# Performance work log

Measured on AMD Instinct MI355X. Metric: run time of the kernel, lower is better.

Reference implementation:

```python
import jax, jax.numpy as jnp
import numpy as np
import itertools

DIM = 7
N_H2, N_H3 = 21, 77

def _perm_sign(p):
    inv = sum(1 for i in range(len(p)) for j in range(i + 1, len(p)) if p[i] > p[j])
    return -1.0 if inv % 2 else 1.0

def _build_wedge_constants():
    # C[a,b,c] = sign of (pair_a, pair_b, triple_c) as a permutation of (0..6),
    # zero unless the 2+2+3 indices are disjoint (coefficient of the volume form
    # in omega_a ^ omega_b ^ Phi_c on ordered-multi-index components).
    idx2 = list(itertools.combinations(range(DIM), 2))   # 21 ordered pairs
    idx3 = list(itertools.combinations(range(DIM), 3))   # 35 ordered triples
    C = np.zeros((len(idx2), len(idx2), len(idx3)), dtype=np.float32)
    for a, pa in enumerate(idx2):
        sa = set(pa)
        for b, pb in enumerate(idx2):
            if sa & set(pb):
                continue
            sab = sa | set(pb)
            for c, pc in enumerate(idx3):
                full = pa + pb + pc
                if sab.isdisjoint(pc):
                    C[a, b, c] = _perm_sign(full)
    return jnp.asarray(C)

C_WEDGE = _build_wedge_constants()  # (21, 21, 35), sparse structure constants

def setup_inputs() -> dict:
    key = jax.random.key(0)
    k1, k2, k3 = jax.random.split(key, 3)
    batch = 4096
    omega = jax.random.normal(k1, (batch, N_H2, 21), dtype=jnp.float32)
    Phi = jax.random.normal(k2, (batch, N_H3, 35), dtype=jnp.float32)
    metric = jax.random.normal(k3, (batch, DIM, DIM), dtype=jnp.float32)
    return {"omega": omega, "Phi": Phi, "metric": metric}

def reference(omega, Phi, metric):
    # Monte-Carlo volume weights, normalized (normalize=True path)
    vol = jnp.sqrt(jnp.abs(jnp.linalg.det(metric)))        # (n,)
    w = vol / vol.sum()
    # Fused triple wedge contraction replacing the 21*21*77 python loops:
    # D[n,i,j,c] = sum_{a,b} C[a,b,c] omega[n,i,a] omega[n,j,b]
    D = jnp.einsum('abc,nia,njb->nijc', C_WEDGE, omega, omega)
    Pw = Phi * w[:, None, None]                             # fold MC weight into Phi
    S = jnp.einsum('nijc,nkc->ijk', D, Pw)                  # (21,21,77), symmetric in i,j
    # Original code writes +integral for j>=i and forces -integral for j<i
    upper = jnp.triu(jnp.ones((N_H2, N_H2), dtype=bool))[:, :, None]
    Y = jnp.where(upper, S, -S)
    # Gram matrix and spectrum
    M = jnp.einsum('ijk,ijl->kl', Y, Y)                     # (77,77)
    eigenvalues = jnp.linalg.eigvalsh(M)[::-1]              # descending, like torch path
    return Y, M, eigenvalues
```

## Files before the change

kernel.cpp:

```cpp
#include <hip/hip_runtime.h>
#include <math.h>

#define NBATCH 4096
#define NH2 21
#define NK 77
#define NC 35
#define NIJ 441
#define Y_SIZE 33957
#define M_SIZE 5929
#define VOLOFF Y_SIZE
#define VSUM (Y_SIZE + 4096)
#define NPAIR 231
#define BLK 512
#define NPB 16
#define GRID_B (NBATCH / NPB)
#define EIGT 640
#define LDS_K 72

#define NSLOT 16
#define SLOT_STRIDE 17792
#define WS2OFF_FB  (NSLOT * SLOT_STRIDE)
#define WS2OFF_PRV (GRID_B * SLOT_STRIDE)
#define WS_NEED_PRV ((size_t)(WS2OFF_PRV + 160) * 4)

#define SZ_OMEGA  (NBATCH * NH2 * NH2)
#define SZ_PHI    (NBATCH * NK * NC)
#define SZ_METRIC (NBATCH * 7 * 7)

struct WTab {
  int a[NC][6];
  int b[NC][6];
  int sg[NC][6];
};

constexpr WTab make_wtab() {
  WTab W{};
  int p0[21] = {}, p1[21] = {};
  int idx = 0;
  for (int x = 0; x < 7; ++x)
    for (int y = x + 1; y < 7; ++y) { p0[idx] = x; p1[idx] = y; ++idx; }
  int t0[35] = {}, t1[35] = {}, t2[35] = {};
  idx = 0;
  for (int x = 0; x < 7; ++x)
    for (int y = x + 1; y < 7; ++y)
      for (int z = y + 1; z < 7; ++z) { t0[idx] = x; t1[idx] = y; t2[idx] = z; ++idx; }
  int cnt[35] = {};
  for (int a = 0; a < 21; ++a)
    for (int b = 0; b < 21; ++b) {
      int pa0 = p0[a], pa1 = p1[a], pb0 = p0[b], pb1 = p1[b];
      if (pa0 == pb0 || pa0 == pb1 || pa1 == pb0 || pa1 == pb1) continue;
      bool used[7] = {};
      used[pa0] = true; used[pa1] = true; used[pb0] = true; used[pb1] = true;
      int tr[3] = {}; int k = 0;
      for (int x = 0; x < 7; ++x) if (!used[x]) tr[k++] = x;
      int c = -1;
      for (int cc = 0; cc < 35; ++cc)
        if (t0[cc] == tr[0] && t1[cc] == tr[1] && t2[cc] == tr[2]) { c = cc; break; }
      int perm[7] = {pa0, pa1, pb0, pb1, tr[0], tr[1], tr[2]};
      int inv = 0;
      for (int i = 0; i < 7; ++i)
        for (int j = i + 1; j < 7; ++j)
          if (perm[i] > perm[j]) ++inv;
      W.a[c][cnt[c]] = a; W.b[c][cnt[c]] = b; W.sg[c][cnt[c]] = (inv & 1) ? -1 : 1;
      ++cnt[c];
    }
  return W;
}

__device__ __forceinline__ int trioff(int i) { return 21 * i - (i * (i - 1)) / 2; }

__device__ __forceinline__ unsigned f2bf(float x) {
  union { float f; unsigned u; } v; v.f = x;
  return ((v.u + 0x7FFFu + ((v.u >> 16) & 1u)) >> 16) & 0xFFFFu;
}

typedef float f32x4 __attribute__((ext_vector_type(4)));
typedef float f32x2 __attribute__((ext_vector_type(2)));
typedef short s16x8 __attribute__((ext_vector_type(8)));

__device__ __forceinline__ f32x2 pk_fma(f32x2 a, f32x2 b, f32x2 c) {
  f32x2 d;
  asm("v_pk_fma_f32 %0, %1, %2, %3" : "=v"(d) : "v"(a), "v"(b), "v"(c));
  return d;
}

template <int CTRL>
__device__ __forceinline__ float dppadd(float x) {
  union { float f; int i; } u, r;
  u.f = x;
  r.i = __builtin_amdgcn_update_dpp(0, u.i, CTRL, 0xF, 0xF, true);
  return x + r.f;
}
__device__ __forceinline__ float oct_sum(float x) {
  x = dppadd<0xB1>(x);
  x = dppadd<0x4E>(x);
  x = dppadd<0x141>(x);
  return x;
}
__device__ __forceinline__ float wave_sum(float x) {
  x = dppadd<0xB1>(x);
  x = dppadd<0x4E>(x);
  x = dppadd<0x141>(x);
  x = dppadd<0x140>(x);
  x = dppadd<0x142>(x);
  x = dppadd<0x143>(x);
  return x;
}
__device__ __forceinline__ float readlane63(float x) {
  union { float f; int i; } u; u.f = x;
  union { int i; float f; } r;
  r.i = __builtin_amdgcn_readlane(u.i, 63);
  return r.f;
}
__device__ __forceinline__ float readlane0(float x) {
  union { float f; int i; } u; u.f = x;
  union { int i; float f; } r;
  r.i = __builtin_amdgcn_readfirstlane(u.i);
  return r.f;
}
__device__ __forceinline__ float readlaneN(float x, int lane) {
  union { float f; int i; } u; u.f = x;
  union { int i; float f; } r;
  r.i = __builtin_amdgcn_readlane(u.i, lane);
  return r.f;
}

__global__ __launch_bounds__(256) void vol_kernel(const float* __restrict__ metric,
                                                  float* __restrict__ out) {
  const int n = blockIdx.x * 256 + threadIdx.x;
  double a[7][7];
#pragma unroll
  for (int r = 0; r < 7; ++r)
#pragma unroll
    for (int c = 0; c < 7; ++c) a[r][c] = (double)metric[n * 49 + r * 7 + c];

  double det = 1.0;
#pragma unroll
  for (int k = 0; k < 7; ++k) {
#pragma unroll
    for (int r = k + 1; r < 7; ++r) {
      bool sw = fabs(a[r][k]) > fabs(a[k][k]);
#pragma unroll
      for (int c = k; c < 7; ++c) {
        double u = a[k][c], v = a[r][c];
        a[k][c] = sw ? v : u;
        a[r][c] = sw ? u : v;
      }
    }
    det *= a[k][k];
    double inv = (a[k][k] != 0.0) ? 1.0 / a[k][k] : 0.0;
#pragma unroll
    for (int r = k + 1; r < 7; ++r) {
      double f = a[r][k] * inv;
#pragma unroll
      for (int c = k + 1; c < 7; ++c) a[r][c] -= f * a[k][c];
    }
  }
  float vol = (float)sqrt(fabs(det));
  out[VOLOFF + n] = vol;

  float s = vol;
#pragma unroll
  for (int off = 32; off > 0; off >>= 1) s += __shfl_down(s, off, 64);
  __shared__ float partial[4];
  const int lane = threadIdx.x & 63, wv = threadIdx.x >> 6;
  if (lane == 0) partial[wv] = s;
  __syncthreads();
  if (threadIdx.x == 0)
    atomicAdd(out + VSUM, partial[0] + partial[1] + partial[2] + partial[3]);
}

__global__ __launch_bounds__(BLK) void contract_kernel(const float* __restrict__ omega,
                                                       const float* __restrict__ Phi,
                                                       const float* __restrict__ out,
                                                       float* __restrict__ wsS,
                                                       const int priv) {
  constexpr WTab W = make_wtab();
  __shared__ __align__(16) short ldsD[256 * LDS_K];
  __shared__ __align__(16) short ldsP[80 * LDS_K];
  __shared__ __align__(16) float ldsO[NH2 * 28];

  const int t = threadIdx.x;
  const int lane = t & 63;
  const int wv = t >> 6;
  const int quad = lane >> 4;
  const int col = lane & 15;
  const int n0 = blockIdx.x * NPB;

  for (int f = t; f < 256 * (LDS_K / 2); f += BLK) ((int*)ldsD)[f] = 0;
  for (int f = t; f < 80 * (LDS_K / 2); f += BLK) ((int*)ldsP)[f] = 0;

  const bool roleA = (t < NPAIR);
  const bool roleB = (t >= 256) && (t < 256 + NPAIR);
  int pi = 0, pj = 0;
  {
    const int p = roleA ? t : (roleB ? (t - 256) : 0);
    int i = 0;
    while (i < 20 && trioff(i + 1) <= p) ++i;
    pi = i;
    pj = p - trioff(i) + i;
  }

  float rA = 0.0f, rB[6], rvn;
  {
    const float* om = omega + n0 * 441;
    const float* ph = Phi + n0 * 2695;
    if (t < 441) rA = om[t];
#pragma unroll
    for (int j = 0; j < 6; ++j) {
      const int e = t + j * BLK;
      rB[j] = (e < 2695) ? ph[e] : 0.0f;
    }
    rvn = out[VOLOFF + n0];
  }

  f32x4 acc[2][5];
#pragma unroll
  for (int mi = 0; mi < 2; ++mi)
#pragma unroll
    for (int nt = 0; nt < 5; ++nt) acc[mi][nt] = (f32x4){0.f, 0.f, 0.f, 0.f};

  for (int it = 0; it < NPB; ++it) {
    __syncthreads();

    if (t < 441) ldsO[(t / 21) * 28 + (t % 21)] = rA;
    {
      const float vn = rvn;
#pragma unroll
      for (int j = 0; j < 6; ++j) {
        const int e = t + j * BLK;
        if (e < 2695) {
          const int q = e / 35, c = e % 35;
          ldsP[q * LDS_K + c] = (short)f2bf(vn * rB[j]);
        }
      }
    }
    __syncthreads();

    if (it + 1 < NPB) {
      const int n1 = n0 + it + 1;
      const float* om2 = omega + n1 * 441;
      const float* ph2 = Phi + n1 * 2695;
      if (t < 441) rA = om2[t];
#pragma unroll
      for (int j = 0; j < 6; ++j) {
        const int e = t + j * BLK;
        if (e < 2695) rB[j] = ph2[e];
      }
      rvn = out[VOLOFF + n1];
    }

    if (roleA || roleB) {
      float wi[21], wj[21];
      const float* oi = ldsO + pi * 28;
      const float* oj = ldsO + pj * 28;
#pragma unroll
      for (int a = 0; a < 20; a += 4) {
        float4 v = *(const float4*)(oi + a);
        wi[a] = v.x; wi[a + 1] = v.y; wi[a + 2] = v.z; wi[a + 3] = v.w;
        float4 u = *(const float4*)(oj + a);
        wj[a] = u.x; wj[a + 1] = u.y; wj[a + 2] = u.z; wj[a + 3] = u.w;
      }
      wi[20] = oi[20]; wj[20] = oj[20];

      if (roleA) {
        float d[18];
#pragma unroll
        for (int c = 0; c < 18; ++c) {
          float dd = 0.0f;
#pragma unroll
          for (int u = 0; u < 6; ++u)
            dd = fmaf((W.sg[c][u] > 0) ? wi[W.a[c][u]] : -wi[W.a[c][u]], wj[W.b[c][u]], dd);
          d[c] = dd;
        }
        int* Drow = (int*)ldsD + t * (LDS_K / 2);
#pragma unroll
        for (int k2 = 0; k2 < 9; ++k2)
          Drow[k2] = (int)(f2bf(d[2 * k2]) | (f2bf(d[2 * k2 + 1]) << 16));
      } else {
        float d[17];
#pragma unroll
        for (int c = 18; c < 35; ++c) {
          float dd = 0.0f;
#pragma unroll
          for (int u = 0; u < 6; ++u)
            dd = fmaf((W.sg[c][u] > 0) ? wi[W.a[c][u]] : -wi[W.a[c][u]], wj[W.b[c][u]], dd);
          d[c - 18] = dd;
        }
        int* Drow = (int*)ldsD + (t - 256) * (LDS_K / 2);
#pragma unroll
        for (int k2 = 0; k2 < 8; ++k2)
          Drow[9 + k2] = (int)(f2bf(d[2 * k2]) | (f2bf(d[2 * k2 + 1]) << 16));
        Drow[17] = (int)f2bf(d[16]);
      }
    }
    __syncthreads();

#pragma unroll
    for (int s = 0; s < 2; ++s) {
      const int kof = s * 32 + quad * 8;
      s16x8 a0 = *(const s16x8*)(ldsD + ((wv * 2 + 0) * 16 + col) * LDS_K + kof);
      s16x8 a1 = *(const s16x8*)(ldsD + ((wv * 2 + 1) * 16 + col) * LDS_K + kof);
      s16x8 b[5];
#pragma unroll
      for (int nt = 0; nt < 5; ++nt)
        b[nt] = *(const s16x8*)(ldsP + (nt * 16 + col) * LDS_K + kof);
#pragma unroll
      for (int nt = 0; nt < 5; ++nt) {
        acc[0][nt] = __builtin_amdgcn_mfma_f32_16x16x32_bf16(a0, b[nt], acc[0][nt], 0, 0, 0);
        acc[1][nt] = __builtin_amdgcn_mfma_f32_16x16x32_bf16(a1, b[nt], acc[1][nt], 0, 0, 0);
      }
    }
  }

  if (priv) {
    float* slot = wsS + (size_t)blockIdx.x * SLOT_STRIDE;
#pragma unroll
    for (int mi = 0; mi < 2; ++mi) {
      const int mt = wv * 2 + mi;
#pragma unroll
      for (int r = 0; r < 4; ++r) {
        const int m = mt * 16 + quad * 4 + r;
        if (m < NPAIR) {
#pragma unroll
          for (int nt = 0; nt < 5; ++nt) {
            const int q = nt * 16 + col;
            if (q < 77) slot[m * NK + q] = acc[mi][nt][r];
          }
        }
      }
    }
  } else {
    float* slot = wsS + (size_t)(blockIdx.x & (NSLOT - 1)) * SLOT_STRIDE;
#pragma unroll
    for (int mi = 0; mi < 2; ++mi) {
      const int mt = wv * 2 + mi;
#pragma unroll
      for (int r = 0; r < 4; ++r) {
        const int m = mt * 16 + quad * 4 + r;
        if (m < NPAIR) {
#pragma unroll
          for (int nt = 0; nt < 5; ++nt) {
            const int q = nt * 16 + col;
            if (q < 77) atomicAdd(&slot[m * NK + q], acc[mi][nt][r]);
          }
        }
      }
    }
  }
}

__global__ __launch_bounds__(256) void finalize_y(const float* __restrict__ wsS,
                                                  float* __restrict__ out,
                                                  const int nslot) {
  const int e = blockIdx.x * 256 + threadIdx.x;
  if (e >= NPAIR * NK) return;
  const int p = e / NK, k = e % NK;
  int i = 0;
  while (i < 20 && trioff(i + 1) <= p) ++i;
  const int j = p - trioff(i) + i;
  float v0 = 0.0f, v1 = 0.0f, v2 = 0.0f, v3 = 0.0f;
  const float* base = wsS + e;
  int s = 0;
#pragma unroll 1
  for (; s + 4 <= nslot; s += 4) {
    v0 += base[(size_t)(s + 0) * SLOT_STRIDE];
    v1 += base[(size_t)(s + 1) * SLOT_STRIDE];
    v2 += base[(size_t)(s + 2) * SLOT_STRIDE];
    v3 += base[(size_t)(s + 3) * SLOT_STRIDE];
  }
  for (; s < nslot; ++s) v0 += base[(size_t)s * SLOT_STRIDE];
  float v = (v0 + v1) + (v2 + v3);
  v *= 1.0f / out[VSUM];
  out[(i * 21 + j) * NK + k] = v;
  if (j != i) out[(j * 21 + i) * NK + k] = -v;
}

__global__ __launch_bounds__(EIGT) void gram_kernel(const float* __restrict__ Y,
                                                    float* __restrict__ Mout) {
  const int k = blockIdx.x;
  const int t = threadIdx.x;
  const int l = t >> 3, s = t & 7;
  float acc = 0.0f;
  if (l < NK) {
    for (int ij = s; ij < NIJ; ij += 8)
      acc = fmaf(Y[ij * NK + k], Y[ij * NK + l], acc);
  }
  acc = oct_sum(acc);
  if (s == 0 && l < NK) Mout[k * NK + l] = acc;
}

__global__ __launch_bounds__(64, 1) void tridiag_kernel(const float* __restrict__ Min,
                                                        float* __restrict__ ws2) {
  const int l = threadIdx.x;
  const int br = l >> 3, bc = l & 7;
  f32x2 A2[10][5];
#pragma unroll
  for (int r = 0; r < 10; ++r) {
    const int g = 10 * br + r;
#pragma unroll
    for (int c2 = 0; c2 < 5; ++c2) {
      const int gc0 = 10 * bc + 2 * c2;
      A2[r][c2][0] = (g < 77 && gc0 < 77) ? Min[g * 77 + gc0] : 0.0f;
      A2[r][c2][1] = (g < 77 && gc0 + 1 < 77) ? Min[g * 77 + gc0 + 1] : 0.0f;
    }
  }

  float rc[10], rr[10];
#pragma unroll
  for (int c2 = 0; c2 < 5; ++c2) {
    rc[2 * c2]     = __shfl(A2[0][c2][0], bc, 64);
    rc[2 * c2 + 1] = __shfl(A2[0][c2][1], bc, 64);
    rr[2 * c2]     = __shfl(A2[0][c2][0], br, 64);
    rr[2 * c2 + 1] = __shfl(A2[0][c2][1], br, 64);
  }

#pragma unroll 1
  for (int kb = 0; kb < 8; ++kb) {
#pragma unroll
    for (int ko = 0; ko < 10; ++ko) {
      if (kb == 7 && ko >= 5) break;
      const int k = kb * 10 + ko;
      const int nko = (ko + 1) % 10;
      const int nkb = kb + (ko == 9 ? 1 : 0);
      const int nic = nkb * 8 + bc, nir = nkb * 8 + br;

      float part = 0.0f;
      if (br == 0) {
#pragma unroll
        for (int c2 = 0; c2 < 5; ++c2) {
          const int gc0 = 10 * bc + 2 * c2;
          const float x0 = rc[2 * c2], xv = rc[2 * c2 + 1];
          part += (gc0 > k) ? x0 * x0 : 0.0f;
          part += (gc0 + 1 > k) ? xv * xv : 0.0f;
        }
      }
      part = oct_sum(part);
      const float sigma2 = readlane0(part);
      if (sigma2 < 1e-26f) {
        if (l == 0) ws2[80 + k] = 0.0f;
#pragma unroll
        for (int c2 = 0; c2 < 5; ++c2) {
          rc[2 * c2]     = __shfl(A2[nko][c2][0], nic, 64);
          rc[2 * c2 + 1] = __shfl(A2[nko][c2][1], nic, 64);
          rr[2 * c2]     = __shfl(A2[nko][c2][0], nir, 64);
          rr[2 * c2 + 1] = __shfl(A2[nko][c2][1], nir, 64);
        }
        continue;
      }
      const float x1 = readlaneN(rc[nko], nkb);
      const float sigma = __builtin_amdgcn_sqrtf(sigma2);
      const float alpha = (x1 >= 0.0f) ? -sigma : sigma;
      const float beta = __builtin_amdgcn_rcpf(fmaf(-alpha, x1, sigma2));
      const float xha = x1 - alpha;
      if (l == 0) ws2[80 + k] = alpha;

      f32x2 vc2[5];
      float vr[10];
#pragma unroll
      for (int c2 = 0; c2 < 5; ++c2) {
        const int gc0 = 10 * bc + 2 * c2;
        vc2[c2][0] = (gc0 > k) ? ((gc0 == k + 1) ? xha : rc[2 * c2]) : 0.0f;
        vc2[c2][1] = (gc0 + 1 > k) ? ((gc0 + 1 == k + 1) ? xha : rc[2 * c2 + 1]) : 0.0f;
        const int gr0 = 10 * br + 2 * c2;
        vr[2 * c2] = (gr0 > k) ? ((gr0 == k + 1) ? xha : rr[2 * c2]) : 0.0f;
        vr[2 * c2 + 1] = (gr0 + 1 > k) ? ((gr0 + 1 == k + 1) ? xha : rr[2 * c2 + 1]) : 0.0f;
      }

      float p[10];
#pragma unroll
      for (int r = 0; r < 10; ++r) {
        f32x2 a = (f32x2){0.f, 0.f};
#pragma unroll
        for (int c2 = 0; c2 < 5; ++c2) a = pk_fma(A2[r][c2], vc2[c2], a);
        p[r] = a[0] + a[1];
      }
#pragma unroll
      for (int r = 0; r < 10; ++r) {
        p[r] = oct_sum(p[r]) * beta;
        p[r] = (10 * br + r > k) ? p[r] : 0.0f;
      }

      f32x2 pc2[5];
#pragma unroll
      for (int c2 = 0; c2 < 5; ++c2) {
        pc2[c2][0] = __shfl(p[2 * c2], 9 * bc, 64);
        pc2[c2][1] = __shfl(p[2 * c2 + 1], 9 * bc, 64);
      }

      float kp = 0.0f;
      if (bc == 0) {
#pragma unroll
        for (int r = 0; r < 10; ++r) kp = fmaf(p[r], vr[r], kp);
      }
      kp = wave_sum(kp);
      const float hb = 0.5f * beta * readlane63(kp);

      float w[10];
#pragma unroll
      for (int r = 0; r < 10; ++r) w[r] = fmaf(-hb, vr[r], p[r]);
      const f32x2 mhb = (f32x2){-hb, -hb};
      f32x2 wc2[5];
#pragma unroll
      for (int c2 = 0; c2 < 5; ++c2) wc2[c2] = pk_fma(mhb, vc2[c2], pc2[c2]);

      {
        const f32x2 nv = (f32x2){-vr[nko], -vr[nko]};
        const f32x2 nw = (f32x2){-w[nko], -w[nko]};
#pragma unroll
        for (int c2 = 0; c2 < 5; ++c2)
          A2[nko][c2] = pk_fma(nv, wc2[c2], pk_fma(nw, vc2[c2], A2[nko][c2]));
      }
#pragma unroll
      for (int c2 = 0; c2 < 5; ++c2) {
        rc[2 * c2]     = __shfl(A2[nko][c2][0], nic, 64);
        rc[2 * c2 + 1] = __shfl(A2[nko][c2][1], nic, 64);
        rr[2 * c2]     = __shfl(A2[nko][c2][0], nir, 64);
        rr[2 * c2 + 1] = __shfl(A2[nko][c2][1], nir, 64);
      }
#pragma unroll
      for (int r = 0; r < 10; ++r) {
        if (r == nko) continue;
        const f32x2 nv = (f32x2){-vr[r], -vr[r]};
        const f32x2 nw = (f32x2){-w[r], -w[r]};
#pragma unroll
        for (int c2 = 0; c2 < 5; ++c2)
          A2[r][c2] = pk_fma(nv, wc2[c2], pk_fma(nw, vc2[c2], A2[r][c2]));
      }
    }
  }

  if (br == bc) {
#pragma unroll
    for (int e = 0; e < 10; ++e)
      ws2[10 * br + e] = (e & 1) ? A2[e][e / 2][1] : A2[e][e / 2][0];
  }
  if (l == 63) ws2[80 + 75] = A2[6][2][1];
}

__global__ __launch_bounds__(EIGT) void bisect_kernel(const float* __restrict__ ws2,
                                                      float* __restrict__ eout) {
  __shared__ float dsh[80], esh[80], e2sh[80];
  __shared__ float red[10], red2[10];
  const int t = threadIdx.x;
  const int lane = t & 63, wv = t >> 6;
  if (t < 80) {
    dsh[t] = ws2[t];
    esh[t] = (t < 76) ? ws2[80 + t] : 0.0f;
  }
  __syncthreads();
  if (t < 76) e2sh[t] = esh[t] * esh[t];

  float lo_ = 1e30f, hi_ = -1e30f;
  if (t < 77) {
    const float r = ((t > 0) ? fabsf(esh[t - 1]) : 0.0f) +
                    ((t < 76) ? fabsf(esh[t]) : 0.0f);
    lo_ = dsh[t] - r;
    hi_ = dsh[t] + r;
  }
#pragma unroll
  for (int off = 1; off < 64; off <<= 1) {
    lo_ = fminf(lo_, __shfl_xor(lo_, off, 64));
    hi_ = fmaxf(hi_, __shfl_xor(hi_, off, 64));
  }
  if (lane == 0) { red[wv] = lo_; red2[wv] = hi_; }
  __syncthreads();
  lo_ = red[0]; hi_ = red2[0];
#pragma unroll
  for (int u = 1; u < 10; ++u) { lo_ = fminf(lo_, red[u]); hi_ = fmaxf(hi_, red2[u]); }
  const float span = hi_ - lo_;
  const float glo = lo_ - 0.001f * span - 1e-6f;
  const float ghi = hi_ + 0.001f * span + 1e-6f;

  {
    const int e = t >> 3;
    const int s = t & 7;
    const int g = (t & 63) >> 3;
    float lo = glo, hi = ghi;
    for (int r = 0; r < 13; ++r) {
      const float step = (hi - lo) * (1.0f / 9.0f);
      const float x = fmaf(step, (float)(s + 1), lo);
      float q = dsh[0] - x;
      int cnt = (q < 0.0f);
#pragma unroll 4
      for (int i = 1; i < 77; ++i) {
        q = (fabsf(q) < 1e-30f) ? -1e-30f : q;
        q = dsh[i] - x - e2sh[i - 1] * __builtin_amdgcn_rcpf(q);
        cnt += (q < 0.0f);
      }
      const unsigned long long mask = __ballot(cnt > e);
      const int b = (int)((mask >> (g * 8)) & 0xFFull);
      const int z = b ? __builtin_ctz(b) : 8;
      const float nlo = fmaf(step, (float)z, lo);
      hi = (z == 8) ? hi : fmaf(step, (float)(z + 1), lo);
      lo = nlo;
    }
    if (s == 0 && e < 77) eout[76 - e] = 0.5f * (lo + hi);
  }
}

extern "C" void kernel_launch(void* const* d_in, const int* in_sizes, int n_in,
                              void* d_out, int out_size, void* d_ws, size_t ws_size,
                              hipStream_t stream) {
  const float* omega  = (const float*)d_in[0];
  const float* Phi    = (const float*)d_in[1];
  const float* metric = (const float*)d_in[2];
  for (int q = 0; q < n_in && q < 3; ++q) {
    if (in_sizes[q] == SZ_OMEGA)       omega  = (const float*)d_in[q];
    else if (in_sizes[q] == SZ_PHI)    Phi    = (const float*)d_in[q];
    else if (in_sizes[q] == SZ_METRIC) metric = (const float*)d_in[q];
  }

  float* out = (float*)d_out;
  float* ws  = (float*)d_ws;

  const int priv = (ws_size >= WS_NEED_PRV) ? 1 : 0;
  const int nslot = priv ? GRID_B : NSLOT;
  float* ws2 = ws + (priv ? WS2OFF_PRV : WS2OFF_FB);

  hipMemsetAsync(d_out, 0, (size_t)out_size * sizeof(float), stream);
  if (!priv)
    hipMemsetAsync(d_ws, 0, (size_t)WS2OFF_FB * sizeof(float), stream);

  hipLaunchKernelGGL(vol_kernel, dim3(NBATCH / 256), dim3(256), 0, stream, metric, out);
  hipLaunchKernelGGL(contract_kernel, dim3(GRID_B), dim3(BLK), 0, stream,
                     omega, Phi, out, ws, priv);
  hipLaunchKernelGGL(finalize_y, dim3((NPAIR * NK + 255) / 256), dim3(256), 0, stream,
                     ws, out, nslot);
  hipLaunchKernelGGL(gram_kernel, dim3(NK), dim3(EIGT), 0, stream,
                     out, out + Y_SIZE);
  hipLaunchKernelGGL(tridiag_kernel, dim3(1), dim3(64), 0, stream,
                     out + Y_SIZE, ws2);
  hipLaunchKernelGGL(bisect_kernel, dim3(1), dim3(EIGT), 0, stream,
                     ws2, out + Y_SIZE + M_SIZE);
}
```

Baseline: 309.7 us.

## Fuse volume determinant into contract kernel and drop output memset

Drops the separate vol_kernel. Each contract block now computes the 7x7 determinants for its own 16 batch elements into LDS and writes one per-block partial volume sum to workspace. finalize_y reduces the 256 partials itself, so the global atomic sum and the full-output memset are no longer needed. This saves a kernel launch and a memset on the critical path, but 16 threads per block now run a serial double-precision elimination before the main loop starts.

```diff
diff --git a/kernel.cpp b/kernel.cpp
--- a/kernel.cpp
+++ b/kernel.cpp
@@ -8,8 +8,6 @@
 #define NIJ 441
 #define Y_SIZE 33957
 #define M_SIZE 5929
-#define VOLOFF Y_SIZE
-#define VSUM (Y_SIZE + 4096)
 #define NPAIR 231
 #define BLK 512
 #define NPB 16
@@ -21,7 +19,7 @@
 #define SLOT_STRIDE 17792
 #define WS2OFF_FB  (NSLOT * SLOT_STRIDE)
 #define WS2OFF_PRV (GRID_B * SLOT_STRIDE)
-#define WS_NEED_PRV ((size_t)(WS2OFF_PRV + 160) * 4)
+#define WS_NEED_PRV ((size_t)(WS2OFF_PRV + 160 + GRID_B) * 4)
 
 #define SZ_OMEGA  (NBATCH * NH2 * NH2)
 #define SZ_PHI    (NBATCH * NK * NC)
@@ -125,60 +123,17 @@
   return r.f;
 }
 
-__global__ __launch_bounds__(256) void vol_kernel(const float* __restrict__ metric,
-                                                  float* __restrict__ out) {
-  const int n = blockIdx.x * 256 + threadIdx.x;
-  double a[7][7];
-#pragma unroll
-  for (int r = 0; r < 7; ++r)
-#pragma unroll
-    for (int c = 0; c < 7; ++c) a[r][c] = (double)metric[n * 49 + r * 7 + c];
-
-  double det = 1.0;
-#pragma unroll
-  for (int k = 0; k < 7; ++k) {
-#pragma unroll
-    for (int r = k + 1; r < 7; ++r) {
-      bool sw = fabs(a[r][k]) > fabs(a[k][k]);
-#pragma unroll
-      for (int c = k; c < 7; ++c) {
-        double u = a[k][c], v = a[r][c];
-        a[k][c] = sw ? v : u;
-        a[r][c] = sw ? u : v;
-      }
-    }
-    det *= a[k][k];
-    double inv = (a[k][k] != 0.0) ? 1.0 / a[k][k] : 0.0;
-#pragma unroll
-    for (int r = k + 1; r < 7; ++r) {
-      double f = a[r][k] * inv;
-#pragma unroll
-      for (int c = k + 1; c < 7; ++c) a[r][c] -= f * a[k][c];
-    }
-  }
-  float vol = (float)sqrt(fabs(det));
-  out[VOLOFF + n] = vol;
-
-  float s = vol;
-#pragma unroll
-  for (int off = 32; off > 0; off >>= 1) s += __shfl_down(s, off, 64);
-  __shared__ float partial[4];
-  const int lane = threadIdx.x & 63, wv = threadIdx.x >> 6;
-  if (lane == 0) partial[wv] = s;
-  __syncthreads();
-  if (threadIdx.x == 0)
-    atomicAdd(out + VSUM, partial[0] + partial[1] + partial[2] + partial[3]);
-}
-
 __global__ __launch_bounds__(BLK) void contract_kernel(const float* __restrict__ omega,
                                                        const float* __restrict__ Phi,
-                                                       const float* __restrict__ out,
+                                                       const float* __restrict__ metric,
                                                        float* __restrict__ wsS,
+                                                       float* __restrict__ vsp,
                                                        const int priv) {
   constexpr WTab W = make_wtab();
   __shared__ __align__(16) short ldsD[256 * LDS_K];
   __shared__ __align__(16) short ldsP[80 * LDS_K];
   __shared__ __align__(16) float ldsO[NH2 * 28];
+  __shared__ float ldsVol[NPB];
 
   const int t = threadIdx.x;
   const int lane = t & 63;
@@ -189,6 +144,45 @@
 
   for (int f = t; f < 256 * (LDS_K / 2); f += BLK) ((int*)ldsD)[f] = 0;
   for (int f = t; f < 80 * (LDS_K / 2); f += BLK) ((int*)ldsP)[f] = 0;
+
+  if (t < NPB) {
+    const int n = n0 + t;
+    double a[7][7];
+#pragma unroll
+    for (int r = 0; r < 7; ++r)
+#pragma unroll
+      for (int c = 0; c < 7; ++c) a[r][c] = (double)metric[n * 49 + r * 7 + c];
+    double det = 1.0;
+#pragma unroll
+    for (int k = 0; k < 7; ++k) {
+#pragma unroll
+      for (int r = k + 1; r < 7; ++r) {
+        bool sw = fabs(a[r][k]) > fabs(a[k][k]);
+#pragma unroll
+        for (int c = k; c < 7; ++c) {
+          double u = a[k][c], v = a[r][c];
+          a[k][c] = sw ? v : u;
+          a[r][c] = sw ? u : v;
+        }
+      }
+      det *= a[k][k];
+      double inv = (a[k][k] != 0.0) ? 1.0 / a[k][k] : 0.0;
+#pragma unroll
+      for (int r = k + 1; r < 7; ++r) {
+        double f = a[r][k] * inv;
+#pragma unroll
+        for (int c = k + 1; c < 7; ++c) a[r][c] -= f * a[k][c];
+      }
+    }
+    ldsVol[t] = (float)sqrt(fabs(det));
+  }
+  __syncthreads();
+  if (t == 0) {
+    float s = 0.0f;
+#pragma unroll
+    for (int i = 0; i < NPB; ++i) s += ldsVol[i];
+    vsp[blockIdx.x] = s;
+  }
 
   const bool roleA = (t < NPAIR);
   const bool roleB = (t >= 256) && (t < 256 + NPAIR);
@@ -211,7 +205,7 @@
       const int e = t + j * BLK;
       rB[j] = (e < 2695) ? ph[e] : 0.0f;
     }
-    rvn = out[VOLOFF + n0];
+    rvn = ldsVol[0];
   }
 
   f32x4 acc[2][5];
@@ -247,7 +241,7 @@
         const int e = t + j * BLK;
         if (e < 2695) rB[j] = ph2[e];
       }
-      rvn = out[VOLOFF + n1];
+      rvn = ldsVol[it + 1];
     }
 
     if (roleA || roleB) {
@@ -351,9 +345,20 @@
 }
 
 __global__ __launch_bounds__(256) void finalize_y(const float* __restrict__ wsS,
+                                                  const float* __restrict__ vsp,
                                                   float* __restrict__ out,
                                                   const int nslot) {
-  const int e = blockIdx.x * 256 + threadIdx.x;
+  __shared__ float vsh[4];
+  const int tt = threadIdx.x;
+  {
+    float pv = vsp[tt];
+    pv = wave_sum(pv);
+    if ((tt & 63) == 63) vsh[tt >> 6] = pv;
+  }
+  __syncthreads();
+  const float vsum = (vsh[0] + vsh[1]) + (vsh[2] + vsh[3]);
+
+  const int e = blockIdx.x * 256 + tt;
   if (e >= NPAIR * NK) return;
   const int p = e / NK, k = e % NK;
   int i = 0;
@@ -371,7 +376,7 @@
   }
   for (; s < nslot; ++s) v0 += base[(size_t)s * SLOT_STRIDE];
   float v = (v0 + v1) + (v2 + v3);
-  v *= 1.0f / out[VSUM];
+  v *= 1.0f / vsum;
   out[(i * 21 + j) * NK + k] = v;
   if (j != i) out[(j * 21 + i) * NK + k] = -v;
 }
@@ -617,16 +622,15 @@
   const int priv = (ws_size >= WS_NEED_PRV) ? 1 : 0;
   const int nslot = priv ? GRID_B : NSLOT;
   float* ws2 = ws + (priv ? WS2OFF_PRV : WS2OFF_FB);
-
-  hipMemsetAsync(d_out, 0, (size_t)out_size * sizeof(float), stream);
+  float* vsp = ws2 + 160;
+
   if (!priv)
     hipMemsetAsync(d_ws, 0, (size_t)WS2OFF_FB * sizeof(float), stream);
 
-  hipLaunchKernelGGL(vol_kernel, dim3(NBATCH / 256), dim3(256), 0, stream, metric, out);
   hipLaunchKernelGGL(contract_kernel, dim3(GRID_B), dim3(BLK), 0, stream,
-                     omega, Phi, out, ws, priv);
+                     omega, Phi, metric, ws, vsp, priv);
   hipLaunchKernelGGL(finalize_y, dim3((NPAIR * NK + 255) / 256), dim3(256), 0, stream,
-                     ws, out, nslot);
+                     ws, vsp, out, nslot);
   hipLaunchKernelGGL(gram_kernel, dim3(NK), dim3(EIGT), 0, stream,
                      out, out + Y_SIZE);
   hipLaunchKernelGGL(tridiag_kernel, dim3(1), dim3(64), 0, stream,
```

Result: no change. 313.9 us (+1.3%).
